# Kernel optimization log

Measured on AMD Instinct MI355X. Metric: run time of the kernel, lower is better.

The kernel has to match this reference:

```python
import jax, jax.numpy as jnp
import numpy as np

TOP_K = 16
MEMORY_SIZE = 256
FEAT_DIM = 512
PROMPT_SHAPE = (64, 2048)
BATCH = 512
EPS = 1e-8  # torch cosine_similarity norm clamp


def setup_inputs() -> dict:
    key = jax.random.key(0)
    k1, k2, k3 = jax.random.split(key, 3)
    features = jax.random.normal(k1, (BATCH, FEAT_DIM), dtype=jnp.float32)
    keys = jax.random.normal(k2, (MEMORY_SIZE, FEAT_DIM), dtype=jnp.float32)
    memory = jax.random.normal(k3, (MEMORY_SIZE,) + PROMPT_SHAPE, dtype=jnp.float32)
    return {"features": features, "keys": keys, "memory": memory}


def reference(features, keys, memory):
    # Cosine similarity of each feature vs every memory key: (B, M)
    f_n = features / jnp.maximum(jnp.linalg.norm(features, axis=-1, keepdims=True), EPS)
    k_n = keys / jnp.maximum(jnp.linalg.norm(keys, axis=-1, keepdims=True), EPS)
    sim = f_n @ k_n.T  # (B, M)

    # top-k per sample, clamp negatives to 0, renormalize
    top_sim, top_ids = jax.lax.top_k(sim, TOP_K)  # (B, K)
    top_sim = jnp.maximum(top_sim, 0.0)
    w = top_sim / jnp.sum(top_sim, axis=-1, keepdims=True)  # (B, K)

    # Weighted gather-sum over memory bank, expressed as sparse-weight GEMM:
    # scatter per-sample weights into a (B, M) matrix, then contract with memory.
    B = w.shape[0]
    W = jnp.zeros((B, MEMORY_SIZE), dtype=w.dtype)
    W = W.at[jnp.arange(B)[:, None], top_ids].add(w)
    ctx = jnp.einsum('bm,mpq->bpq', W, memory)  # (B, 64, 2048)
    return ctx
```

## Files before the change

kernel.cpp:

```cpp
#include <hip/hip_runtime.h>

#define FEAT   512
#define MEMN   256
#define BATCH  512
#define PROMPT 131072
#define TOPK   16
#define EPSF   1e-8f

#define CCOLS  32
#define NCH    32
#define NGRP   128
#define BT     64
#define NTILE  8

__global__ __launch_bounds__(256) void knorm_kernel(
    const float* __restrict__ keys, float* __restrict__ kn)
{
    __shared__ float red[4];
    const int m = blockIdx.x;
    const int tid = threadIdx.x;
    float2 v = *reinterpret_cast<const float2*>(keys + m * FEAT + tid * 2);
    float p = v.x * v.x + v.y * v.y;
    for (int off = 32; off; off >>= 1) p += __shfl_down(p, off);
    if ((tid & 63) == 0) red[tid >> 6] = p;
    __syncthreads();
    float s = red[0] + red[1] + red[2] + red[3];
    float nrm = sqrtf(s); if (nrm < EPSF) nrm = EPSF;
    const float inv = 1.0f / nrm;
    float2 o; o.x = v.x * inv; o.y = v.y * inv;
    *reinterpret_cast<float2*>(kn + m * FEAT + tid * 2) = o;
}

__global__ __launch_bounds__(256) void topk_kernel(
    const float* __restrict__ features,
    const float* __restrict__ kn,
    int* __restrict__ out_ids,
    float* __restrict__ out_w)
{
    __shared__ float f_lds[FEAT];
    __shared__ float sim_lds[MEMN];
    __shared__ float red[4];

    const int b = blockIdx.x;
    const int tid = threadIdx.x;

    float2 fv = *reinterpret_cast<const float2*>(features + b * FEAT + tid * 2);
    *reinterpret_cast<float2*>(f_lds + tid * 2) = fv;
    float p = fv.x * fv.x + fv.y * fv.y;
    for (int off = 32; off; off >>= 1) p += __shfl_down(p, off);
    if ((tid & 63) == 0) red[tid >> 6] = p;
    __syncthreads();
    const float f2 = red[0] + red[1] + red[2] + red[3];
    float fn = sqrtf(f2); if (fn < EPSF) fn = EPSF;
    const float invf = 1.0f / fn;

    const int wave = tid >> 6, lane = tid & 63;
    const int jc = lane & 15, msub = lane >> 4;
    for (int pss = 0; pss < 16; ++pss) {
        const int m = pss * 16 + wave * 4 + msub;
        const float* krow = kn + m * FEAT;
        float dot = 0.f;
#pragma unroll
        for (int s = 0; s < 8; ++s) {
            float4 kv = *reinterpret_cast<const float4*>(krow + s * 64 + jc * 4);
            float4 fw = *reinterpret_cast<const float4*>(f_lds + s * 64 + jc * 4);
            dot += kv.x * fw.x + kv.y * fw.y + kv.z * fw.z + kv.w * fw.w;
        }
        dot += __shfl_xor(dot, 1); dot += __shfl_xor(dot, 2);
        dot += __shfl_xor(dot, 4); dot += __shfl_xor(dot, 8);
        if (jc == 0) sim_lds[m] = dot * invf;
    }
    __syncthreads();

    if (tid < 64) {
        const int lane_ = tid;
        float v0 = sim_lds[lane_];
        float v1 = sim_lds[lane_ + 64];
        float v2 = sim_lds[lane_ + 128];
        float v3 = sim_lds[lane_ + 192];
        int myid = 0;

        for (int r = 0; r < TOPK; ++r) {
            float bv = v0; int bi = lane_;
            if (v1 > bv) { bv = v1; bi = lane_ + 64;  }
            if (v2 > bv) { bv = v2; bi = lane_ + 128; }
            if (v3 > bv) { bv = v3; bi = lane_ + 192; }
            for (int off = 32; off > 0; off >>= 1) {
                const float ov = __shfl_down(bv, off);
                const int   oi = __shfl_down(bi, off);
                if (ov > bv || (ov == bv && oi < bi)) { bv = ov; bi = oi; }
            }
            bi = __shfl(bi, 0);
            if (lane_ == r) myid = bi;
            if ((bi & 63) == lane_) {
                const int slot = bi >> 6;
                if      (slot == 0) v0 = -1e30f;
                else if (slot == 1) v1 = -1e30f;
                else if (slot == 2) v2 = -1e30f;
                else                v3 = -1e30f;
            }
        }

        if (lane_ < TOPK) {
            float val = sim_lds[myid];
            if (val < 0.f) val = 0.f;
            float s = val;
            for (int off = 1; off < TOPK; off <<= 1)
                s += __shfl_xor(s, off);
            out_ids[b * TOPK + lane_] = myid;
            out_w[b * TOPK + lane_]   = val / s;
        }
    }
}

__global__ __launch_bounds__(256, 4) void ctx_kernel(
    const float* __restrict__ mem,
    const int* __restrict__ ids,
    const float* __restrict__ wgt,
    float* __restrict__ out)
{
    __shared__ float slab[MEMN * CCOLS];

    const int bid  = blockIdx.x;
    const int xcd  = bid & 7;
    const int idx  = bid >> 3;
    const int tile = idx >> 4;
    const int g    = xcd * 16 + (idx & 15);
    const int b_base = tile * BT;
    const int col0   = g * (NCH * CCOLS);

    const int tid  = threadIdx.x;
    const int wave = tid >> 6, lane = tid & 63;
    const int bg   = lane >> 3;
    const int cg   = lane & 7;

    const int b0 = b_base + wave * 16 + bg;
    const int b1 = b0 + 8;

    int   off0[TOPK], off1[TOPK];
    float w0[TOPK],  w1[TOPK];
#pragma unroll
    for (int q = 0; q < 4; ++q) {
        int4   i0 = *reinterpret_cast<const int4*>(ids + b0 * TOPK + q * 4);
        int4   i1 = *reinterpret_cast<const int4*>(ids + b1 * TOPK + q * 4);
        float4 v0 = *reinterpret_cast<const float4*>(wgt + b0 * TOPK + q * 4);
        float4 v1 = *reinterpret_cast<const float4*>(wgt + b1 * TOPK + q * 4);
        off0[q*4+0] = i0.x * (CCOLS*4) + cg * 16;
        off0[q*4+1] = i0.y * (CCOLS*4) + cg * 16;
        off0[q*4+2] = i0.z * (CCOLS*4) + cg * 16;
        off0[q*4+3] = i0.w * (CCOLS*4) + cg * 16;
        off1[q*4+0] = i1.x * (CCOLS*4) + cg * 16;
        off1[q*4+1] = i1.y * (CCOLS*4) + cg * 16;
        off1[q*4+2] = i1.z * (CCOLS*4) + cg * 16;
        off1[q*4+3] = i1.w * (CCOLS*4) + cg * 16;
        w0[q*4+0] = v0.x; w0[q*4+1] = v0.y; w0[q*4+2] = v0.z; w0[q*4+3] = v0.w;
        w1[q*4+0] = v1.x; w1[q*4+1] = v1.y; w1[q*4+2] = v1.z; w1[q*4+3] = v1.w;
    }

    const char* slb = reinterpret_cast<const char*>(slab);

    for (int c = 0; c < NCH; ++c) {
        const int cb = col0 + c * CCOLS;

#pragma unroll
        for (int i = 0; i < 8; ++i) {
            const int r = wave * 64 + i * 8 + bg;
            const float* gp = mem + (size_t)r * PROMPT + cb + cg * 4;
            float* lp = slab + (size_t)(wave * 64 + i * 8) * CCOLS + lane * 4;
            __builtin_amdgcn_global_load_lds(
                (const __attribute__((address_space(1))) unsigned int*)gp,
                (__attribute__((address_space(3))) unsigned int*)lp,
                16, 0, 0);
        }
        __syncthreads();

        float4 acc;
        acc.x = acc.y = acc.z = acc.w = 0.f;
#pragma unroll
        for (int k = 0; k < TOPK; ++k) {
            const float4 v = *reinterpret_cast<const float4*>(slb + off0[k]);
            acc.x += w0[k] * v.x; acc.y += w0[k] * v.y;
            acc.z += w0[k] * v.z; acc.w += w0[k] * v.w;
        }
        *reinterpret_cast<float4*>(out + (size_t)b0 * PROMPT + cb + cg * 4) = acc;

        acc.x = acc.y = acc.z = acc.w = 0.f;
#pragma unroll
        for (int k = 0; k < TOPK; ++k) {
            const float4 v = *reinterpret_cast<const float4*>(slb + off1[k]);
            acc.x += w1[k] * v.x; acc.y += w1[k] * v.y;
            acc.z += w1[k] * v.z; acc.w += w1[k] * v.w;
        }
        *reinterpret_cast<float4*>(out + (size_t)b1 * PROMPT + cb + cg * 4) = acc;

        __syncthreads();
    }
}

extern "C" void kernel_launch(void* const* d_in, const int* in_sizes, int n_in,
                              void* d_out, int out_size, void* d_ws, size_t ws_size,
                              hipStream_t stream) {
    const float* features = (const float*)d_in[0];
    const float* keys     = (const float*)d_in[1];
    const float* mem      = (const float*)d_in[2];
    float* out = (float*)d_out;

    char* ws = (char*)d_ws;
    int*   ids = (int*)ws;
    float* wgt = (float*)(ws + 32768);
    float* kn  = (float*)(ws + 65536);

    knorm_kernel<<<MEMN, 256, 0, stream>>>(keys, kn);
    topk_kernel<<<BATCH, 256, 0, stream>>>(features, kn, ids, wgt);
    ctx_kernel<<<NTILE * NGRP, 256, 0, stream>>>(mem, ids, wgt, out);
}
```

Measured before the change: 555.7 us.

## Double-buffer memory slabs in LDS and double the batch tile per block

The ctx kernel now stages memory column chunks into two LDS buffers. The next chunk's global-to-LDS loads overlap with the weighted gather-sum on the current chunk, with manual vmcnt waits and barriers between them. Each block also covers 128 batch rows instead of 64, with each thread computing four outputs, so each memory slab is loaded from global memory half as often. The costs are 64KB of LDS per block, occupancy capped at two blocks per CU, and more registers for the 64 offsets and 64 weights.

```diff
diff --git a/kernel.cpp b/kernel.cpp
--- a/kernel.cpp
+++ b/kernel.cpp
@@ -10,8 +10,8 @@
 #define CCOLS  32
 #define NCH    32
 #define NGRP   128
-#define BT     64
-#define NTILE  8
+#define BT     128
+#define NTILE  4
 
 __global__ __launch_bounds__(256) void knorm_kernel(
     const float* __restrict__ keys, float* __restrict__ kn)
@@ -113,13 +113,14 @@
     }
 }
 
-__global__ __launch_bounds__(256, 4) void ctx_kernel(
+__global__ __launch_bounds__(256, 2) void ctx_kernel(
     const float* __restrict__ mem,
     const int* __restrict__ ids,
     const float* __restrict__ wgt,
     float* __restrict__ out)
 {
-    __shared__ float slab[MEMN * CCOLS];
+    __shared__ float slab0[MEMN * CCOLS];
+    __shared__ float slab1[MEMN * CCOLS];
 
     const int bid  = blockIdx.x;
     const int xcd  = bid & 7;
@@ -134,66 +135,76 @@
     const int bg   = lane >> 3;
     const int cg   = lane & 7;
 
-    const int b0 = b_base + wave * 16 + bg;
-    const int b1 = b0 + 8;
-
-    int   off0[TOPK], off1[TOPK];
-    float w0[TOPK],  w1[TOPK];
+    const int bA = b_base + wave * 8 + bg;
+
+    int   off[4 * TOPK];
+    float w[4 * TOPK];
 #pragma unroll
     for (int q = 0; q < 4; ++q) {
-        int4   i0 = *reinterpret_cast<const int4*>(ids + b0 * TOPK + q * 4);
-        int4   i1 = *reinterpret_cast<const int4*>(ids + b1 * TOPK + q * 4);
-        float4 v0 = *reinterpret_cast<const float4*>(wgt + b0 * TOPK + q * 4);
-        float4 v1 = *reinterpret_cast<const float4*>(wgt + b1 * TOPK + q * 4);
-        off0[q*4+0] = i0.x * (CCOLS*4) + cg * 16;
-        off0[q*4+1] = i0.y * (CCOLS*4) + cg * 16;
-        off0[q*4+2] = i0.z * (CCOLS*4) + cg * 16;
-        off0[q*4+3] = i0.w * (CCOLS*4) + cg * 16;
-        off1[q*4+0] = i1.x * (CCOLS*4) + cg * 16;
-        off1[q*4+1] = i1.y * (CCOLS*4) + cg * 16;
-        off1[q*4+2] = i1.z * (CCOLS*4) + cg * 16;
-        off1[q*4+3] = i1.w * (CCOLS*4) + cg * 16;
-        w0[q*4+0] = v0.x; w0[q*4+1] = v0.y; w0[q*4+2] = v0.z; w0[q*4+3] = v0.w;
-        w1[q*4+0] = v1.x; w1[q*4+1] = v1.y; w1[q*4+2] = v1.z; w1[q*4+3] = v1.w;
-    }
-
-    const char* slb = reinterpret_cast<const char*>(slab);
-
-    for (int c = 0; c < NCH; ++c) {
-        const int cb = col0 + c * CCOLS;
-
+        const int b = bA + q * 32;
+#pragma unroll
+        for (int r = 0; r < 4; ++r) {
+            int4   iv = *reinterpret_cast<const int4*>(ids + b * TOPK + r * 4);
+            float4 wv = *reinterpret_cast<const float4*>(wgt + b * TOPK + r * 4);
+            off[q*16 + r*4 + 0] = iv.x * (CCOLS*4) + cg * 16;
+            off[q*16 + r*4 + 1] = iv.y * (CCOLS*4) + cg * 16;
+            off[q*16 + r*4 + 2] = iv.z * (CCOLS*4) + cg * 16;
+            off[q*16 + r*4 + 3] = iv.w * (CCOLS*4) + cg * 16;
+            w[q*16 + r*4 + 0] = wv.x; w[q*16 + r*4 + 1] = wv.y;
+            w[q*16 + r*4 + 2] = wv.z; w[q*16 + r*4 + 3] = wv.w;
+        }
+    }
+
+    auto stage = [&](float* buf, int cb) {
 #pragma unroll
         for (int i = 0; i < 8; ++i) {
             const int r = wave * 64 + i * 8 + bg;
             const float* gp = mem + (size_t)r * PROMPT + cb + cg * 4;
-            float* lp = slab + (size_t)(wave * 64 + i * 8) * CCOLS + lane * 4;
+            float* lp = buf + (wave * 64 + i * 8) * CCOLS + lane * 4;
             __builtin_amdgcn_global_load_lds(
                 (const __attribute__((address_space(1))) unsigned int*)gp,
                 (__attribute__((address_space(3))) unsigned int*)lp,
                 16, 0, 0);
         }
-        __syncthreads();
-
-        float4 acc;
-        acc.x = acc.y = acc.z = acc.w = 0.f;
-#pragma unroll
-        for (int k = 0; k < TOPK; ++k) {
-            const float4 v = *reinterpret_cast<const float4*>(slb + off0[k]);
-            acc.x += w0[k] * v.x; acc.y += w0[k] * v.y;
-            acc.z += w0[k] * v.z; acc.w += w0[k] * v.w;
-        }
-        *reinterpret_cast<float4*>(out + (size_t)b0 * PROMPT + cb + cg * 4) = acc;
-
-        acc.x = acc.y = acc.z = acc.w = 0.f;
-#pragma unroll
-        for (int k = 0; k < TOPK; ++k) {
-            const float4 v = *reinterpret_cast<const float4*>(slb + off1[k]);
-            acc.x += w1[k] * v.x; acc.y += w1[k] * v.y;
-            acc.z += w1[k] * v.z; acc.w += w1[k] * v.w;
-        }
-        *reinterpret_cast<float4*>(out + (size_t)b1 * PROMPT + cb + cg * 4) = acc;
-
-        __syncthreads();
+    };
+
+    auto compute = [&](const float* buf, int cb) {
+        const char* slb = reinterpret_cast<const char*>(buf);
+#pragma unroll
+        for (int q = 0; q < 4; ++q) {
+            float4 acc;
+            acc.x = acc.y = acc.z = acc.w = 0.f;
+#pragma unroll
+            for (int k = 0; k < TOPK; ++k) {
+                const float4 v = *reinterpret_cast<const float4*>(slb + off[q*16 + k]);
+                const float ww = w[q*16 + k];
+                acc.x += ww * v.x; acc.y += ww * v.y;
+                acc.z += ww * v.z; acc.w += ww * v.w;
+            }
+            const int b = bA + q * 32;
+            *reinterpret_cast<float4*>(out + (size_t)b * PROMPT + cb + cg * 4) = acc;
+        }
+    };
+
+    stage(slab0, col0);
+    asm volatile("s_waitcnt vmcnt(0)" ::: "memory");
+    __builtin_amdgcn_s_barrier();
+    asm volatile("" ::: "memory");
+
+    for (int c = 0; c < NCH; c += 2) {
+        stage(slab1, col0 + (c + 1) * CCOLS);
+        asm volatile("" ::: "memory");
+        compute(slab0, col0 + c * CCOLS);
+        asm volatile("s_waitcnt vmcnt(4)" ::: "memory");
+        __builtin_amdgcn_s_barrier();
+        asm volatile("" ::: "memory");
+
+        if (c + 2 < NCH) stage(slab0, col0 + (c + 2) * CCOLS);
+        asm volatile("" ::: "memory");
+        compute(slab1, col0 + (c + 1) * CCOLS);
+        asm volatile("s_waitcnt vmcnt(4)" ::: "memory");
+        __builtin_amdgcn_s_barrier();
+        asm volatile("" ::: "memory");
     }
 }
 
```

New measurement: 469.6 us. -15.5%, faster.
